# Kernel tuning notes

Measured on AMD Instinct MI355X. Metric: run time of the kernel, lower is better.

Reference implementation:

```python
import jax, jax.numpy as jnp
import numpy as np

EMBED_DIM = 1024
NUM_HEADS = 16
HEAD_DIM = EMBED_DIM // NUM_HEADS


def setup_inputs() -> dict:
    key = jax.random.key(0)
    ks = jax.random.split(key, 11)
    L, N, E = 2048, 2, EMBED_DIM
    S = 2048
    def xavier(k, shape):
        fan_in, fan_out = shape[1], shape[0]
        limit = float(np.sqrt(6.0 / (fan_in + fan_out)))
        return jax.random.uniform(k, shape, jnp.float32, -limit, limit)
    return {
        "query": jax.random.normal(ks[0], (L, N, E), jnp.float32),
        "key": jax.random.normal(ks[1], (S, N, E), jnp.float32),
        "value": jax.random.normal(ks[2], (S, N, E), jnp.float32),
        "Wq": xavier(ks[3], (E, E)), "bq": jnp.zeros((E,), jnp.float32),
        "Wk": xavier(ks[4], (E, E)), "bk": jnp.zeros((E,), jnp.float32),
        "Wv": xavier(ks[5], (E, E)), "bv": jnp.zeros((E,), jnp.float32),
        "Wo": xavier(ks[6], (E, E)), "bo": jnp.zeros((E,), jnp.float32),
    }


def reference(query, key, value, Wq, bq, Wk, bk, Wv, bv, Wo, bo):
    # query/key/value: [L, N, E] (seq-first, batch_first=False)
    L, N, E = query.shape
    S = key.shape[0]
    H, D = NUM_HEADS, HEAD_DIM
    q = query @ Wq.T + bq   # [L, N, E]
    k = key @ Wk.T + bk     # [S, N, E]
    v = value @ Wv.T + bv   # [S, N, E]
    # [L, N*H, D] -> [N*H, L, D]
    q = q.reshape(L, N * H, D).transpose(1, 0, 2)
    k = k.reshape(S, N * H, D).transpose(1, 0, 2)
    v = v.reshape(S, N * H, D).transpose(1, 0, 2)
    scores = jnp.einsum("bld,bsd->bls", q, k) / jnp.sqrt(jnp.float32(D))  # [N*H, L, S]
    attn = jax.nn.softmax(scores, axis=-1)  # dropout p=0.0 -> identity
    out = jnp.einsum("bls,bsd->bld", attn, v)  # [N*H, L, D]
    out = out.transpose(1, 0, 2).reshape(L, N, E)
    attn_output = out @ Wo.T + bo  # [L, N, E]
    # need_weights=True, average_attn_weights=True
    attn_weights = attn.reshape(N, H, L, S).mean(axis=1)  # [N, L, S]
    return attn_output, attn_weights
```

## Files before the change

kernel.cpp:

```cpp
#include <hip/hip_runtime.h>

#define EDIM 1024
#define LSEQ 2048
#define NBATCH 2
#define NHEADS 16
#define HDIM 64
#define QSCALE 0.18033688011112042f

typedef unsigned short us;
typedef __attribute__((ext_vector_type(8))) short short8;
typedef __attribute__((ext_vector_type(4))) float floatx4;
typedef __attribute__((ext_vector_type(16))) float floatx16;

#define MFMA16(a, b, c) __builtin_amdgcn_mfma_f32_16x16x32_bf16((a), (b), (c), 0, 0, 0)
#define MFMA32(a, b, c) __builtin_amdgcn_mfma_f32_32x32x16_bf16((a), (b), (c), 0, 0, 0)
#define ZERO16 ((floatx16){0.f,0.f,0.f,0.f,0.f,0.f,0.f,0.f,0.f,0.f,0.f,0.f,0.f,0.f,0.f,0.f})

#define WAIT_VM4 asm volatile("s_waitcnt vmcnt(4)" ::: "memory")
#define WAIT_VM0 asm volatile("s_waitcnt vmcnt(0)" ::: "memory")
#define WAIT_LGKM0 asm volatile("s_waitcnt lgkmcnt(0)" ::: "memory")
#define CFENCE asm volatile("" ::: "memory")

__device__ __forceinline__ us f2bf(float f) {
  unsigned int u = __float_as_uint(f);
  u += 0x7fffu + ((u >> 16) & 1u);
  return (us)(u >> 16);
}

__device__ __forceinline__ void gload16(const void* g, void* l) {
  __builtin_amdgcn_global_load_lds((const __attribute__((address_space(1))) unsigned int*)g,
                                   (__attribute__((address_space(3))) unsigned int*)l, 16, 0, 0);
}

__device__ __forceinline__ unsigned int cvtpk(float lo, float hi_) {
  unsigned int r;
  asm("v_cvt_pk_bf16_f32 %0, %1, %2" : "=v"(r) : "v"(lo), "v"(hi_));
  return r;
}
__device__ __forceinline__ void plswap(unsigned int& a, unsigned int& b) {
  asm("v_permlane32_swap_b32 %0, %1" : "+v"(a), "+v"(b));
}
__device__ __forceinline__ short8 mkfrag(unsigned int a, unsigned int b, unsigned int c,
                                         unsigned int d) {
  union { unsigned int u[4]; short8 v; } x;
  x.u[0] = a; x.u[1] = b; x.u[2] = c; x.u[3] = d;
  return x.v;
}
__device__ __forceinline__ void pack2(const floatx16 p, short8& f0, short8& f1) {
  unsigned int A = cvtpk(p[0], p[1]), B = cvtpk(p[4], p[5]); plswap(A, B);
  unsigned int C = cvtpk(p[2], p[3]), D = cvtpk(p[6], p[7]); plswap(C, D);
  f0 = mkfrag(A, C, B, D);
  unsigned int E = cvtpk(p[8], p[9]), F = cvtpk(p[12], p[13]); plswap(E, F);
  unsigned int G = cvtpk(p[10], p[11]), H = cvtpk(p[14], p[15]); plswap(G, H);
  f1 = mkfrag(E, G, F, H);
}

__global__ void k_f2bf_all(const float* q, const float* k, const float* v,
                           const float* wq, const float* wk, const float* wv, const float* wo,
                           us* dq, us* dk, us* dv, us* dwq, us* dwk, us* dwv, us* dwo) {
  const int z = blockIdx.y;
  const float* s; us* d; int n8;
  if (z == 0)      { s = q;  d = dq;  n8 = 524288; }
  else if (z == 1) { s = k;  d = dk;  n8 = 524288; }
  else if (z == 2) { s = v;  d = dv;  n8 = 524288; }
  else if (z == 3) { s = wq; d = dwq; n8 = 131072; }
  else if (z == 4) { s = wk; d = dwk; n8 = 131072; }
  else if (z == 5) { s = wv; d = dwv; n8 = 131072; }
  else             { s = wo; d = dwo; n8 = 131072; }
  int i = blockIdx.x * blockDim.x + threadIdx.x;
  int stride = gridDim.x * blockDim.x;
  for (; i < n8; i += stride) {
    float4 a = ((const float4*)s)[2 * i];
    float4 b = ((const float4*)s)[2 * i + 1];
    union { us u[8]; uint4 vv; } o;
    o.u[0] = f2bf(a.x); o.u[1] = f2bf(a.y); o.u[2] = f2bf(a.z); o.u[3] = f2bf(a.w);
    o.u[4] = f2bf(b.x); o.u[5] = f2bf(b.y); o.u[6] = f2bf(b.z); o.u[7] = f2bf(b.w);
    ((uint4*)d)[i] = o.vv;
  }
}

template <int MODE>
__device__ __forceinline__ void gemm_core(us* pool,
                                          const us* __restrict__ A, const us* __restrict__ B,
                                          const float* __restrict__ bias, void* __restrict__ outp,
                                          int row0, int col0, float scale) {
  us* const Asb[2] = {pool, pool + 8192};
  us* const Bsb[2] = {pool + 4096, pool + 12288};
  const int t = threadIdx.x;
  const int w = t >> 6, lane = t & 63;
  const int g = lane >> 4, lr = lane & 15;
  const int wm = (w & 1) * 64, wn = (w >> 1) * 64;
  const int srow = lane >> 2, scol = (lane & 3) * 8;
  const int cA = 2 * w;
  const us* Asrc = A + (size_t)(row0 + cA * 16 + srow) * EDIM + scol;
  const us* Bsrc = B + (size_t)(col0 + cA * 16 + srow) * EDIM + scol;

  floatx4 acc[4][4];
#pragma unroll
  for (int mi = 0; mi < 4; ++mi)
#pragma unroll
    for (int ni = 0; ni < 4; ++ni) acc[mi][ni] = (floatx4){0.f, 0.f, 0.f, 0.f};

  auto stage = [&](int kt, int b) {
    const int k0 = kt * 32;
    gload16(Asrc + k0, Asb[b] + cA * 512);
    gload16(Asrc + 16 * EDIM + k0, Asb[b] + cA * 512 + 512);
    gload16(Bsrc + k0, Bsb[b] + cA * 512);
    gload16(Bsrc + 16 * EDIM + k0, Bsb[b] + cA * 512 + 512);
  };

  stage(0, 0);
  stage(1, 1);

  for (int kt = 0; kt < 32; ++kt) {
    if (kt < 31) { WAIT_VM4; } else { WAIT_VM0; }
    __builtin_amdgcn_s_barrier();
    CFENCE;
    const us* Ac = Asb[kt & 1];
    const us* Bc = Bsb[kt & 1];
    short8 af[4], bfr[4];
#pragma unroll
    for (int mi = 0; mi < 4; ++mi) af[mi] = *(const short8*)&Ac[(wm + mi * 16 + lr) * 32 + g * 8];
#pragma unroll
    for (int ni = 0; ni < 4; ++ni) bfr[ni] = *(const short8*)&Bc[(wn + ni * 16 + lr) * 32 + g * 8];
#pragma unroll
    for (int mi = 0; mi < 4; ++mi)
#pragma unroll
      for (int ni = 0; ni < 4; ++ni) acc[mi][ni] = MFMA16(af[mi], bfr[ni], acc[mi][ni]);
    WAIT_LGKM0;
    __builtin_amdgcn_s_barrier();
    CFENCE;
    if (kt + 2 < 32) stage(kt + 2, kt & 1);
  }

  if (MODE == 1) {
    us* Ct = pool;
#pragma unroll
    for (int ni = 0; ni < 4; ++ni) {
      const int colloc = wn + ni * 16 + lr;
      const float bv = bias[col0 + colloc];
#pragma unroll
      for (int mi = 0; mi < 4; ++mi) {
        const int b = wm + mi * 16 + 4 * g;
        unsigned int lo = (unsigned int)f2bf(acc[mi][ni][0] + bv) |
                          ((unsigned int)f2bf(acc[mi][ni][2] + bv) << 16);
        unsigned int hi = (unsigned int)f2bf(acc[mi][ni][1] + bv) |
                          ((unsigned int)f2bf(acc[mi][ni][3] + bv) << 16);
        *(unsigned int*)&Ct[colloc * 136 + (b >> 1)] = lo;
        *(unsigned int*)&Ct[colloc * 136 + 64 + (b >> 1)] = hi;
      }
    }
    __syncthreads();
    const int rr = t >> 1, half = t & 1;
    const int c = col0 + rr, h = c >> 6, d = c & 63;
    us* dst = (us*)outp + (((size_t)half * NHEADS + h) * HDIM + d) * LSEQ + (row0 >> 1);
    const us* srcRow = &Ct[rr * 136 + half * 64];
#pragma unroll
    for (int j = 0; j < 8; ++j)
      *(uint4*)(dst + j * 8) = *(const uint4*)(srcRow + j * 8);
  } else {
#pragma unroll
    for (int ni = 0; ni < 4; ++ni) {
      const int col = col0 + wn + ni * 16 + lr;
      const float bv = bias[col];
#pragma unroll
      for (int mi = 0; mi < 4; ++mi) {
#pragma unroll
        for (int i = 0; i < 4; ++i) {
          const int row = row0 + wm + mi * 16 + g * 4 + i;
          const float v = (acc[mi][ni][i] + bv) * scale;
          if (MODE == 2) {
            ((float*)outp)[(size_t)row * EDIM + col] = v;
          } else {
            const int n = row & 1, sq = row >> 1;
            const int h = col >> 6, d = col & 63;
            ((us*)outp)[(((size_t)n * NHEADS + h) * LSEQ + sq) * HDIM + d] = f2bf(v);
          }
        }
      }
    }
  }
}

__global__ __launch_bounds__(256) void k_gemm_qkv(
    const us* __restrict__ Xq, const us* __restrict__ Xk, const us* __restrict__ Xv,
    const us* __restrict__ Wqb, const us* __restrict__ Wkb, const us* __restrict__ Wvb,
    const float* __restrict__ bq, const float* __restrict__ bk, const float* __restrict__ bv,
    us* __restrict__ qo, us* __restrict__ ko, us* __restrict__ vo) {
  __shared__ us pool[17408];
  const int z = blockIdx.z;
  if (z == 0)      gemm_core<0>(pool, Xq, Wqb, bq, qo, blockIdx.x * 128, blockIdx.y * 128, QSCALE);
  else if (z == 1) gemm_core<0>(pool, Xk, Wkb, bk, ko, blockIdx.x * 128, blockIdx.y * 128, 1.0f);
  else             gemm_core<1>(pool, Xv, Wvb, bv, vo, blockIdx.x * 128, blockIdx.y * 128, 1.0f);
}

__global__ __launch_bounds__(256) void k_gemm_o(const us* __restrict__ A, const us* __restrict__ B,
                                                const float* __restrict__ bias, float* __restrict__ out) {
  __shared__ us pool[16384];
  gemm_core<2>(pool, A, B, bias, out, blockIdx.x * 128, blockIdx.y * 128, 1.0f);
}

__global__ __launch_bounds__(256) void k_attn(const us* __restrict__ qb, const us* __restrict__ kb,
                                              const us* __restrict__ vt, float* __restrict__ rell,
                                              us* __restrict__ O) {
  __shared__ us Ks[2][4096];
  __shared__ us Vs[2][4096];
  __shared__ float elt[4][32];
  const int bh = blockIdx.x;
  const int l0 = blockIdx.y * 128;
  const int t = threadIdx.x, w = t >> 6, lane = t & 63;
  const int ql = lane & 31, hi = lane >> 5;

  short8 qf[4];
  {
    const us* qptr = qb + ((size_t)bh * LSEQ + l0 + w * 32 + ql) * HDIM + hi * 8;
#pragma unroll
    for (int dt = 0; dt < 4; ++dt) qf[dt] = *(const short8*)(qptr + dt * 16);
  }

  int off0[4], off1[4];
#pragma unroll
  for (int j = 0; j < 4; ++j) {
    off0[j] = ql * 64 + (((2 * j + hi) ^ (ql & 7)) << 3);
    off1[j] = (32 + ql) * 64 + (((2 * j + hi) ^ (ql & 7)) << 3);
  }

  const int j0 = 2 * w, j1 = 2 * w + 1;
  const int srA = lane >> 3;
  const int scA = ((lane & 7) ^ (lane >> 3)) * 8;
  const us* Kbase = kb + (size_t)bh * LSEQ * HDIM;
  const us* Vbase = vt + (size_t)bh * HDIM * LSEQ;
  const us* Ksrc0 = Kbase + (j0 * 8 + srA) * HDIM + scA;
  const us* Ksrc1 = Kbase + (j1 * 8 + srA) * HDIM + scA;
  const us* Vsrc0 = Vbase + (size_t)(j0 * 8 + srA) * LSEQ + scA;
  const us* Vsrc1 = Vbase + (size_t)(j1 * 8 + srA) * LSEQ + scA;

  floatx16 oacc0 = ZERO16, oacc1 = ZERO16;
  float ellacc = 0.f;

  auto stageKV = [&](int kt, int b) {
    const int so = kt * 64;
    gload16(Ksrc0 + so * HDIM, &Ks[b][j0 * 512]);
    gload16(Ksrc1 + so * HDIM, &Ks[b][j1 * 512]);
    gload16(Vsrc0 + so, &Vs[b][j0 * 512]);
    gload16(Vsrc1 + so, &Vs[b][j1 * 512]);
  };

  stageKV(0, 0);
  stageKV(1, 1);

  for (int it = 0; it < 32; ++it) {
    if (it < 31) { WAIT_VM4; } else { WAIT_VM0; }
    __builtin_amdgcn_s_barrier();
    CFENCE;
    const us* Kc = Ks[it & 1];
    const us* Vc = Vs[it & 1];

    floatx16 acc0 = ZERO16, acc1 = ZERO16;
    __builtin_amdgcn_s_setprio(1);
#pragma unroll
    for (int dt = 0; dt < 4; ++dt) {
      acc0 = MFMA32(*(const short8*)&Kc[off0[dt]], qf[dt], acc0);
      acc1 = MFMA32(*(const short8*)&Kc[off1[dt]], qf[dt], acc1);
    }
    __builtin_amdgcn_s_setprio(0);
#pragma unroll
    for (int r = 0; r < 16; ++r) {
      acc0[r] = __builtin_amdgcn_exp2f(acc0[r]); ellacc += acc0[r];
      acc1[r] = __builtin_amdgcn_exp2f(acc1[r]); ellacc += acc1[r];
    }
    short8 pa0, pa1, pa2, pa3;
    pack2(acc0, pa0, pa1);
    pack2(acc1, pa2, pa3);
    __builtin_amdgcn_s_setprio(1);
#pragma unroll
    for (int dt2 = 0; dt2 < 2; ++dt2) {
      floatx16& oa = dt2 ? oacc1 : oacc0;
      const int* off = dt2 ? off1 : off0;
      oa = MFMA32(pa0, *(const short8*)&Vc[off[0]], oa);
      oa = MFMA32(pa1, *(const short8*)&Vc[off[1]], oa);
      oa = MFMA32(pa2, *(const short8*)&Vc[off[2]], oa);
      oa = MFMA32(pa3, *(const short8*)&Vc[off[3]], oa);
    }
    __builtin_amdgcn_s_setprio(0);
    WAIT_LGKM0;
    __builtin_amdgcn_s_barrier();
    CFENCE;
    if (it + 2 < 32) stageKV(it + 2, it & 1);
  }

  const float elltot = ellacc + __shfl_xor(ellacc, 32);
  if (lane < 32) {
    const float r0 = 1.0f / elltot;
    elt[w][lane] = r0;
    rell[(size_t)bh * LSEQ + l0 + w * 32 + lane] = r0;
  }
  const int n = bh >> 4, hh = bh & 15;
  us* obase = O + (size_t)n * EDIM + (size_t)hh * HDIM;
#pragma unroll
  for (int r = 0; r < 16; ++r) {
    const int q = (r & 3) + 8 * (r >> 2) + 4 * hi;
    const float rl = elt[w][q];
    const size_t l = l0 + w * 32 + q;
    obase[l * (NBATCH * EDIM) + ql] = f2bf(oacc0[r] * rl);
    obase[l * (NBATCH * EDIM) + 32 + ql] = f2bf(oacc1[r] * rl);
  }
}

__global__ __launch_bounds__(256, 2) void k_weights(const us* __restrict__ qb, const us* __restrict__ kb,
                                                    const float* __restrict__ rell,
                                                    float* __restrict__ Wout) {
  __shared__ us Ks[2][4096];
  const int l0 = blockIdx.x * 256;
  const int s0 = blockIdx.y * 64;
  const int n = blockIdx.z;
  const int t = threadIdx.x, w = t >> 6, lane = t & 63;
  const int ql = lane & 31, hi = lane >> 5;
  const int lbase = l0 + w * 64;
  const int j0 = 2 * w, j1 = 2 * w + 1;
  const int srA = lane >> 3;
  const int scA = ((lane & 7) ^ (lane >> 3)) * 8;
  const us* Kb0 = kb + ((size_t)(n * NHEADS) * LSEQ + s0 + j0 * 8 + srA) * HDIM + scA;
  const us* Kb1 = kb + ((size_t)(n * NHEADS) * LSEQ + s0 + j1 * 8 + srA) * HDIM + scA;

  int off0[4], off1[4];
#pragma unroll
  for (int j = 0; j < 4; ++j) {
    off0[j] = ql * 64 + (((2 * j + hi) ^ (ql & 7)) << 3);
    off1[j] = (32 + ql) * 64 + (((2 * j + hi) ^ (ql & 7)) << 3);
  }

  floatx16 wa00 = ZERO16, wa01 = ZERO16, wa10 = ZERO16, wa11 = ZERO16;

  gload16(Kb0, &Ks[0][j0 * 512]); gload16(Kb1, &Ks[0][j1 * 512]);

  short8 qc0[4], qc1[4];
  float rlc0, rlc1;
  {
    const us* qp0 = qb + ((size_t)(n * NHEADS) * LSEQ + lbase + ql) * HDIM + hi * 8;
    const us* qp1 = qp0 + 32 * HDIM;
#pragma unroll
    for (int dt = 0; dt < 4; ++dt) {
      qc0[dt] = *(const short8*)(qp0 + dt * 16);
      qc1[dt] = *(const short8*)(qp1 + dt * 16);
    }
    rlc0 = rell[(size_t)(n * NHEADS) * LSEQ + lbase + ql];
    rlc1 = rell[(size_t)(n * NHEADS) * LSEQ + lbase + 32 + ql];
  }
  __syncthreads();

  for (int h = 0; h < NHEADS; ++h) {
    const int cur = h & 1;
    short8 qn0[4], qn1[4];
    float rln0 = 0.f, rln1 = 0.f;
    if (h < NHEADS - 1) {
      us* Kn2 = Ks[cur ^ 1];
      gload16(Kb0 + (size_t)(h + 1) * LSEQ * HDIM, Kn2 + j0 * 512);
      gload16(Kb1 + (size_t)(h + 1) * LSEQ * HDIM, Kn2 + j1 * 512);
      const us* qp0 = qb + ((size_t)(n * NHEADS + h + 1) * LSEQ + lbase + ql) * HDIM + hi * 8;
      const us* qp1 = qp0 + 32 * HDIM;
#pragma unroll
      for (int dt = 0; dt < 4; ++dt) {
        qn0[dt] = *(const short8*)(qp0 + dt * 16);
        qn1[dt] = *(const short8*)(qp1 + dt * 16);
      }
      rln0 = rell[(size_t)(n * NHEADS + h + 1) * LSEQ + lbase + ql];
      rln1 = rell[(size_t)(n * NHEADS + h + 1) * LSEQ + lbase + 32 + ql];
    }
    const us* Kc = Ks[cur];
    short8 kf0[4], kf1[4];
#pragma unroll
    for (int dt = 0; dt < 4; ++dt) {
      kf0[dt] = *(const short8*)&Kc[off0[dt]];
      kf1[dt] = *(const short8*)&Kc[off1[dt]];
    }
    {
      floatx16 aA = ZERO16, aB = ZERO16;
#pragma unroll
      for (int dt = 0; dt < 4; ++dt) {
        aA = MFMA32(kf0[dt], qc0[dt], aA);
        aB = MFMA32(kf1[dt], qc0[dt], aB);
      }
#pragma unroll
      for (int r = 0; r < 16; ++r) {
        wa00[r] += __builtin_amdgcn_exp2f(aA[r]) * rlc0;
        wa01[r] += __builtin_amdgcn_exp2f(aB[r]) * rlc0;
      }
    }
    {
      floatx16 cA = ZERO16, cB = ZERO16;
#pragma unroll
      for (int dt = 0; dt < 4; ++dt) {
        cA = MFMA32(kf0[dt], qc1[dt], cA);
        cB = MFMA32(kf1[dt], qc1[dt], cB);
      }
#pragma unroll
      for (int r = 0; r < 16; ++r) {
        wa10[r] += __builtin_amdgcn_exp2f(cA[r]) * rlc1;
        wa11[r] += __builtin_amdgcn_exp2f(cB[r]) * rlc1;
      }
    }
#pragma unroll
    for (int dt = 0; dt < 4; ++dt) { qc0[dt] = qn0[dt]; qc1[dt] = qn1[dt]; }
    rlc0 = rln0; rlc1 = rln1;
    __syncthreads();
  }

  float* wb0 = Wout + (size_t)n * LSEQ * LSEQ + (size_t)(lbase + ql) * LSEQ + s0;
  float* wb1 = Wout + (size_t)n * LSEQ * LSEQ + (size_t)(lbase + 32 + ql) * LSEQ + s0;
#pragma unroll
  for (int r = 0; r < 16; ++r) {
    const int cr = (r & 3) + 8 * (r >> 2) + 4 * hi;
    wb0[cr] = wa00[r] * 0.0625f;
    wb0[32 + cr] = wa01[r] * 0.0625f;
    wb1[cr] = wa10[r] * 0.0625f;
    wb1[32 + cr] = wa11[r] * 0.0625f;
  }
}

extern "C" void kernel_launch(void* const* d_in, const int* in_sizes, int n_in,
                              void* d_out, int out_size, void* d_ws, size_t ws_size,
                              hipStream_t stream) {
  const float* query = (const float*)d_in[0];
  const float* key   = (const float*)d_in[1];
  const float* value = (const float*)d_in[2];
  const float* Wq = (const float*)d_in[3]; const float* bq = (const float*)d_in[4];
  const float* Wk = (const float*)d_in[5]; const float* bk = (const float*)d_in[6];
  const float* Wv = (const float*)d_in[7]; const float* bv = (const float*)d_in[8];
  const float* Wo = (const float*)d_in[9]; const float* bo = (const float*)d_in[10];

  const size_t MB = 1u << 20;
  char* ws = (char*)d_ws;
  us* Xq  = (us*)(ws + 0 * MB);
  us* Xk  = (us*)(ws + 8 * MB);
  us* Xv  = (us*)(ws + 16 * MB);
  us* Wqb = (us*)(ws + 24 * MB);
  us* Wkb = (us*)(ws + 26 * MB);
  us* Wvb = (us*)(ws + 28 * MB);
  us* Wob = (us*)(ws + 30 * MB);
  us* qbuf = (us*)(ws + 32 * MB);
  us* kbuf = (us*)(ws + 40 * MB);
  us* Vt   = (us*)(ws + 48 * MB);
  us* Obuf = (us*)(ws + 56 * MB);
  float* rell = (float*)(ws + 64 * MB);

  k_f2bf_all<<<dim3(256, 7), 256, 0, stream>>>(query, key, value, Wq, Wk, Wv, Wo,
                                               Xq, Xk, Xv, Wqb, Wkb, Wvb, Wob);

  k_gemm_qkv<<<dim3(32, 8, 3), 256, 0, stream>>>(Xq, Xk, Xv, Wqb, Wkb, Wvb, bq, bk, bv,
                                                 qbuf, kbuf, Vt);

  k_attn<<<dim3(32, 16), 256, 0, stream>>>(qbuf, kbuf, Vt, rell, Obuf);

  k_gemm_o<<<dim3(32, 8), 256, 0, stream>>>(Obuf, Wob, bo, (float*)d_out);
  k_weights<<<dim3(8, 32, 2), 256, 0, stream>>>(qbuf, kbuf, rell, (float*)d_out + 4194304);
}
```

Baseline: 156.7 us.

## Halve attention block size and compute softmax row sums with MFMA

The attention kernel now uses 2 waves (64 query rows) per block instead of 4, which doubles the grid to 1024 blocks, and each wave stages twice as many K/V chunks. Row-sum accumulation of the exponentials moves from scalar adds plus a cross-lane shuffle to extra MFMAs against a ones fragment. That removes the shared-memory normalizer table and its LDS round trip. In exchange, K/V reuse per block drops (more global/L2 traffic per query), and the sums are now taken over bf16-rounded probabilities.

```diff
diff --git a/kernel.cpp b/kernel.cpp
--- a/kernel.cpp
+++ b/kernel.cpp
@@ -16,6 +16,7 @@
 #define MFMA32(a, b, c) __builtin_amdgcn_mfma_f32_32x32x16_bf16((a), (b), (c), 0, 0, 0)
 #define ZERO16 ((floatx16){0.f,0.f,0.f,0.f,0.f,0.f,0.f,0.f,0.f,0.f,0.f,0.f,0.f,0.f,0.f,0.f})
 
+#define WAIT_VM8 asm volatile("s_waitcnt vmcnt(8)" ::: "memory")
 #define WAIT_VM4 asm volatile("s_waitcnt vmcnt(4)" ::: "memory")
 #define WAIT_VM0 asm volatile("s_waitcnt vmcnt(0)" ::: "memory")
 #define WAIT_LGKM0 asm volatile("s_waitcnt lgkmcnt(0)" ::: "memory")
@@ -53,6 +54,13 @@
   unsigned int E = cvtpk(p[8], p[9]), F = cvtpk(p[12], p[13]); plswap(E, F);
   unsigned int G = cvtpk(p[10], p[11]), H = cvtpk(p[14], p[15]); plswap(G, H);
   f1 = mkfrag(E, G, F, H);
+}
+
+__device__ __forceinline__ short8 onesfrag() {
+  union { us u[8]; short8 v; } x;
+#pragma unroll
+  for (int i = 0; i < 8; ++i) x.u[i] = 0x3F80;
+  return x.v;
 }
 
 __global__ void k_f2bf_all(const float* q, const float* k, const float* v,
@@ -200,20 +208,20 @@
   gemm_core<2>(pool, A, B, bias, out, blockIdx.x * 128, blockIdx.y * 128, 1.0f);
 }
 
-__global__ __launch_bounds__(256) void k_attn(const us* __restrict__ qb, const us* __restrict__ kb,
+__global__ __launch_bounds__(128) void k_attn(const us* __restrict__ qb, const us* __restrict__ kb,
                                               const us* __restrict__ vt, float* __restrict__ rell,
                                               us* __restrict__ O) {
   __shared__ us Ks[2][4096];
   __shared__ us Vs[2][4096];
-  __shared__ float elt[4][32];
   const int bh = blockIdx.x;
-  const int l0 = blockIdx.y * 128;
+  const int l0 = blockIdx.y * 64;
   const int t = threadIdx.x, w = t >> 6, lane = t & 63;
   const int ql = lane & 31, hi = lane >> 5;
+  const int lbase = l0 + w * 32;
 
   short8 qf[4];
   {
-    const us* qptr = qb + ((size_t)bh * LSEQ + l0 + w * 32 + ql) * HDIM + hi * 8;
+    const us* qptr = qb + ((size_t)bh * LSEQ + lbase + ql) * HDIM + hi * 8;
 #pragma unroll
     for (int dt = 0; dt < 4; ++dt) qf[dt] = *(const short8*)(qptr + dt * 16);
   }
@@ -225,32 +233,36 @@
     off1[j] = (32 + ql) * 64 + (((2 * j + hi) ^ (ql & 7)) << 3);
   }
 
-  const int j0 = 2 * w, j1 = 2 * w + 1;
   const int srA = lane >> 3;
   const int scA = ((lane & 7) ^ (lane >> 3)) * 8;
   const us* Kbase = kb + (size_t)bh * LSEQ * HDIM;
   const us* Vbase = vt + (size_t)bh * HDIM * LSEQ;
-  const us* Ksrc0 = Kbase + (j0 * 8 + srA) * HDIM + scA;
-  const us* Ksrc1 = Kbase + (j1 * 8 + srA) * HDIM + scA;
-  const us* Vsrc0 = Vbase + (size_t)(j0 * 8 + srA) * LSEQ + scA;
-  const us* Vsrc1 = Vbase + (size_t)(j1 * 8 + srA) * LSEQ + scA;
-
-  floatx16 oacc0 = ZERO16, oacc1 = ZERO16;
-  float ellacc = 0.f;
+  const us* Ksrc[4];
+  const us* Vsrc[4];
+#pragma unroll
+  for (int i = 0; i < 4; ++i) {
+    const int jj = 4 * w + i;
+    Ksrc[i] = Kbase + (jj * 8 + srA) * HDIM + scA;
+    Vsrc[i] = Vbase + (size_t)(jj * 8 + srA) * LSEQ + scA;
+  }
+
+  floatx16 oacc0 = ZERO16, oacc1 = ZERO16, ellmf = ZERO16;
+  const short8 onesf = onesfrag();
 
   auto stageKV = [&](int kt, int b) {
     const int so = kt * 64;
-    gload16(Ksrc0 + so * HDIM, &Ks[b][j0 * 512]);
-    gload16(Ksrc1 + so * HDIM, &Ks[b][j1 * 512]);
-    gload16(Vsrc0 + so, &Vs[b][j0 * 512]);
-    gload16(Vsrc1 + so, &Vs[b][j1 * 512]);
+#pragma unroll
+    for (int i = 0; i < 4; ++i) {
+      gload16(Ksrc[i] + so * HDIM, &Ks[b][(4 * w + i) * 512]);
+      gload16(Vsrc[i] + so, &Vs[b][(4 * w + i) * 512]);
+    }
   };
 
   stageKV(0, 0);
   stageKV(1, 1);
 
   for (int it = 0; it < 32; ++it) {
-    if (it < 31) { WAIT_VM4; } else { WAIT_VM0; }
+    if (it < 31) { WAIT_VM8; } else { WAIT_VM0; }
     __builtin_amdgcn_s_barrier();
     CFENCE;
     const us* Kc = Ks[it & 1];
@@ -266,8 +278,8 @@
     __builtin_amdgcn_s_setprio(0);
 #pragma unroll
     for (int r = 0; r < 16; ++r) {
-      acc0[r] = __builtin_amdgcn_exp2f(acc0[r]); ellacc += acc0[r];
-      acc1[r] = __builtin_amdgcn_exp2f(acc1[r]); ellacc += acc1[r];
+      acc0[r] = __builtin_amdgcn_exp2f(acc0[r]);
+      acc1[r] = __builtin_amdgcn_exp2f(acc1[r]);
     }
     short8 pa0, pa1, pa2, pa3;
     pack2(acc0, pa0, pa1);
@@ -282,6 +294,10 @@
       oa = MFMA32(pa2, *(const short8*)&Vc[off[2]], oa);
       oa = MFMA32(pa3, *(const short8*)&Vc[off[3]], oa);
     }
+    ellmf = MFMA32(pa0, onesf, ellmf);
+    ellmf = MFMA32(pa1, onesf, ellmf);
+    ellmf = MFMA32(pa2, onesf, ellmf);
+    ellmf = MFMA32(pa3, onesf, ellmf);
     __builtin_amdgcn_s_setprio(0);
     WAIT_LGKM0;
     __builtin_amdgcn_s_barrier();
@@ -289,21 +305,24 @@
     if (it + 2 < 32) stageKV(it + 2, it & 1);
   }
 
-  const float elltot = ellacc + __shfl_xor(ellacc, 32);
-  if (lane < 32) {
-    const float r0 = 1.0f / elltot;
-    elt[w][lane] = r0;
-    rell[(size_t)bh * LSEQ + l0 + w * 32 + lane] = r0;
+  float rinv[16];
+#pragma unroll
+  for (int r = 0; r < 16; ++r) rinv[r] = 1.0f / ellmf[r];
+  if (ql == 0) {
+#pragma unroll
+    for (int r = 0; r < 16; ++r) {
+      const int q = (r & 3) + 8 * (r >> 2) + 4 * hi;
+      rell[(size_t)bh * LSEQ + lbase + q] = rinv[r];
+    }
   }
   const int n = bh >> 4, hh = bh & 15;
   us* obase = O + (size_t)n * EDIM + (size_t)hh * HDIM;
 #pragma unroll
   for (int r = 0; r < 16; ++r) {
     const int q = (r & 3) + 8 * (r >> 2) + 4 * hi;
-    const float rl = elt[w][q];
-    const size_t l = l0 + w * 32 + q;
-    obase[l * (NBATCH * EDIM) + ql] = f2bf(oacc0[r] * rl);
-    obase[l * (NBATCH * EDIM) + 32 + ql] = f2bf(oacc1[r] * rl);
+    const size_t l = lbase + q;
+    obase[l * (NBATCH * EDIM) + ql] = f2bf(oacc0[r] * rinv[r]);
+    obase[l * (NBATCH * EDIM) + 32 + ql] = f2bf(oacc1[r] * rinv[r]);
   }
 }
 
@@ -450,7 +469,7 @@
   k_gemm_qkv<<<dim3(32, 8, 3), 256, 0, stream>>>(Xq, Xk, Xv, Wqb, Wkb, Wvb, bq, bk, bv,
                                                  qbuf, kbuf, Vt);
 
-  k_attn<<<dim3(32, 16), 256, 0, stream>>>(qbuf, kbuf, Vt, rell, Obuf);
+  k_attn<<<dim3(32, 32), 128, 0, stream>>>(qbuf, kbuf, Vt, rell, Obuf);
 
   k_gemm_o<<<dim3(32, 8), 256, 0, stream>>>(Obuf, Wob, bo, (float*)d_out);
   k_weights<<<dim3(8, 32, 2), 256, 0, stream>>>(qbuf, kbuf, rell, (float*)d_out + 4194304);
```

Result: slower. 164.4 us (+4.9%).
